# Kernel optimization log

Measured on AMD Instinct MI355X. Metric: run time of the kernel, lower is better.

## Reference

```python
import jax, jax.numpy as jnp
import numpy as np

N = 50000          # nodes
E = 500000         # edges
EMB = 64           # hidden_size
R = 2              # DDE num_rounds
RR = 2             # DDE num_reverse_rounds
PRED_IN = 4 * EMB + 4 + 4 * (R + RR)  # 276


def setup_inputs() -> dict:
    key = jax.random.key(0)
    ks = jax.random.split(key, 10)
    x = jax.random.normal(ks[0], (N, EMB), jnp.float32)
    edge_index = jax.random.randint(ks[1], (2, E), 0, N, dtype=jnp.int64)
    edge_attr = jax.random.normal(ks[2], (E, EMB), jnp.float32)
    topic_signal = jax.random.uniform(ks[3], (N, 2), dtype=jnp.float32)
    q_emb = jax.random.normal(ks[4], (E, EMB), jnp.float32)
    # learned parameters
    non_text_emb = jax.random.normal(ks[5], (1, EMB), jnp.float32)
    W1 = jax.random.normal(ks[6], (PRED_IN, EMB), jnp.float32) / np.sqrt(PRED_IN)
    b1 = jnp.zeros((EMB,), jnp.float32)
    W2 = jax.random.normal(ks[7], (EMB, 1), jnp.float32) / np.sqrt(EMB)
    b2 = jnp.zeros((1,), jnp.float32)
    return dict(x=x, edge_index=edge_index, edge_attr=edge_attr,
                topic_signal=topic_signal, q_emb=q_emb,
                non_text_emb=non_text_emb, W1=W1, b1=b1, W2=W2, b2=b2)


def _segment_mean(data, seg, num_segments):
    # mean aggregation as in PyG MessagePassing(aggr='mean'); empty segments -> 0
    s = jax.ops.segment_sum(data, seg, num_segments=num_segments)
    cnt = jax.ops.segment_sum(jnp.ones((seg.shape[0],), data.dtype), seg,
                              num_segments=num_segments)
    return s / jnp.maximum(cnt, 1.0)[:, None]


def reference(x, edge_index, edge_attr, topic_signal, q_emb,
              non_text_emb, W1, b1, W2, b2):
    src, dst = edge_index[0], edge_index[1]
    # replace all-zero node rows with the learned non-text entity embedding
    zero_mask = jnp.all(x == 0, axis=1)
    x = jnp.where(zero_mask[:, None], non_text_emb[0], x)

    feats = [x, topic_signal]  # topic_pe = True
    # DDE forward rounds: aggregate src -> dst along edge_index
    h = topic_signal
    for _ in range(R):
        h = _segment_mean(h[src], dst, N)
        feats.append(h)
    # DDE reverse rounds: flipped edges (dst -> src)
    h = topic_signal
    for _ in range(RR):
        h = _segment_mean(h[dst], src, N)
        feats.append(h)

    h_e = jnp.concatenate(feats, axis=1)                      # [N, EMB+2+2*(R+RR)]
    h_triple = jnp.concatenate([q_emb, h_e[src], edge_attr, h_e[dst]], axis=1)  # [E, PRED_IN]
    hidden = jax.nn.relu(h_triple @ W1 + b1)                  # [E, EMB]
    return (hidden @ W2 + b2).squeeze(-1)                     # [E]
```

## Files before the change

kernel.cpp:

```cpp
#include <hip/hip_runtime.h>
#include <cstdint>
#include <cstddef>


typedef __bf16 bf16x8 __attribute__((ext_vector_type(8)));
typedef float f32x4 __attribute__((ext_vector_type(4)));

__device__ __forceinline__ unsigned int f2bf1(float f) {
    unsigned int u = __float_as_uint(f);
    return (u + 0x7fffu + ((u >> 16) & 1u)) >> 16;
}
__device__ __forceinline__ unsigned int pk2(float a, float b) {
    return f2bf1(a) | (f2bf1(b) << 16);
}
__device__ __forceinline__ bf16x8 cvt8v(float4 a, float4 b) {
    bf16x8 r;
    r[0] = (__bf16)a.x; r[1] = (__bf16)a.y; r[2] = (__bf16)a.z; r[3] = (__bf16)a.w;
    r[4] = (__bf16)b.x; r[5] = (__bf16)b.y; r[6] = (__bf16)b.z; r[7] = (__bf16)b.w;
    return r;
}

#define GL16(gp, lp)                                                        \
    __builtin_amdgcn_global_load_lds(                                       \
        (const __attribute__((address_space(1))) void*)(gp),                \
        (__attribute__((address_space(3))) void*)(lp), 16, 0, 0)


__global__ void k_detect(const int* __restrict__ idx, int E, int* __restrict__ flag) {
    int e = blockIdx.x * blockDim.x + threadIdx.x;
    bool nz = (e < E) && (idx[2 * e + 1] != 0);
    unsigned long long m = __ballot(nz);
    if (m != 0ull && (threadIdx.x & 63) == 0) atomicOr(flag, 1);
}

__global__ void k_convert(const int* __restrict__ idx, int E, const int* __restrict__ flag,
                          int* __restrict__ src_i, int* __restrict__ dst_i,
                          int* __restrict__ cnt_dst, int* __restrict__ cnt_src,
                          unsigned short* __restrict__ pos_f, unsigned short* __restrict__ pos_r) {
    int e = blockIdx.x * blockDim.x + threadIdx.x;
    if (e >= E) return;
    int s, d;
    if (*flag) { s = idx[e];     d = idx[E + e]; }
    else       { s = idx[2 * e]; d = idx[2 * E + 2 * e]; }
    src_i[e] = s; dst_i[e] = d;
    pos_f[e] = (unsigned short)atomicAdd(&cnt_dst[d], 1);
    pos_r[e] = (unsigned short)atomicAdd(&cnt_src[s], 1);
}

__global__ void k_scan(const int* __restrict__ cnt_dst, const int* __restrict__ cnt_src,
                       int* __restrict__ off_f, int* __restrict__ off_r, int N) {
    const int* cnt = (blockIdx.x == 0) ? cnt_dst : cnt_src;
    int* off       = (blockIdx.x == 0) ? off_f   : off_r;
    const int t = threadIdx.x;
    const int C = (N + 1023) / 1024;
    int lo = t * C, hi = lo + C; if (hi > N) hi = N; if (lo > N) lo = N;
    int sum = 0;
    for (int i = lo; i < hi; ++i) sum += cnt[i];
    __shared__ int wsum[16];
    int lane = t & 63, wv = t >> 6;
    int v = sum;
    for (int ofs = 1; ofs < 64; ofs <<= 1) {
        int u = __shfl_up(v, ofs);
        if (lane >= ofs) v += u;
    }
    if (lane == 63) wsum[wv] = v;
    __syncthreads();
    if (wv == 0) {
        int x = (lane < 16) ? wsum[lane] : 0;
        for (int ofs = 1; ofs < 16; ofs <<= 1) {
            int u = __shfl_up(x, ofs);
            if (lane >= ofs) x += u;
        }
        if (lane < 16) wsum[lane] = x;
    }
    __syncthreads();
    int base = (wv > 0 ? wsum[wv - 1] : 0) + (v - sum);
    for (int i = lo; i < hi; ++i) { off[i] = base; base += cnt[i]; }
}

__global__ void k_fill(const int* __restrict__ src_i, const int* __restrict__ dst_i,
                       const unsigned short* __restrict__ pos_f, const unsigned short* __restrict__ pos_r,
                       const int* __restrict__ off_f, const int* __restrict__ off_r,
                       int* __restrict__ csr_f, int* __restrict__ csr_r, int E) {
    int e = blockIdx.x * blockDim.x + threadIdx.x;
    if (e >= E) return;
    int s = src_i[e], d = dst_i[e];
    csr_f[off_f[d] + pos_f[e]] = s;
    csr_r[off_r[s] + pos_r[e]] = d;
}

__global__ void k_round(const int* __restrict__ off_f, const int* __restrict__ csr_f,
                        const int* __restrict__ off_r, const int* __restrict__ csr_r,
                        const float* __restrict__ hf_in,
                        const float* __restrict__ hr_in,
                        float* __restrict__ f_out, float* __restrict__ r_out,
                        int N, int E) {
    int gid = blockIdx.x * blockDim.x + threadIdx.x;
    if (gid >= 2 * N) return;
    const bool rev = gid >= N;
    const int n = rev ? gid - N : gid;
    const int* __restrict__ off = rev ? off_r : off_f;
    const int* __restrict__ csr = rev ? csr_r : csr_f;
    const float2* __restrict__ h = (const float2*)(rev ? hr_in : hf_in);
    float2* __restrict__ o = (float2*)(rev ? r_out : f_out);
    int b = off[n], e = (n + 1 < N) ? off[n + 1] : E;
    float sx = 0.f, sy = 0.f;
    for (int j = b; j < e; ++j) { float2 t = h[csr[j]]; sx += t.x; sy += t.y; }
    float inv = 1.0f / (float)max(e - b, 1);
    o[n] = make_float2(sx * inv, sy * inv);
}

__global__ void k_build(const float* __restrict__ x, const float* __restrict__ topic,
                        const float* __restrict__ nte,
                        const float* __restrict__ f1, const float* __restrict__ f2,
                        const float* __restrict__ r1, const float* __restrict__ r2,
                        unsigned short* __restrict__ he, int N) {
    int n = blockIdx.x * blockDim.x + threadIdx.x;
    if (n >= N) return;
    const float4* xr = (const float4*)(x + (size_t)n * 64);
    float4 v[16];
    bool allz = true;
#pragma unroll
    for (int i = 0; i < 16; ++i) {
        v[i] = xr[i];
        allz = allz && (v[i].x == 0.f && v[i].y == 0.f && v[i].z == 0.f && v[i].w == 0.f);
    }
    const float4* nr = (const float4*)nte;
    unsigned int row[40];
#pragma unroll
    for (int i = 0; i < 16; ++i) {
        float4 s = allz ? nr[i] : v[i];
        row[2 * i]     = pk2(s.x, s.y);
        row[2 * i + 1] = pk2(s.z, s.w);
    }
    row[32] = pk2(topic[2 * n], topic[2 * n + 1]);
    row[33] = pk2(f1[2 * n], f1[2 * n + 1]);
    row[34] = pk2(f2[2 * n], f2[2 * n + 1]);
    row[35] = pk2(r1[2 * n], r1[2 * n + 1]);
    row[36] = pk2(r2[2 * n], r2[2 * n + 1]);
    row[37] = 0u; row[38] = 0u; row[39] = 0u;
    uint4* dst = (uint4*)(he + (size_t)n * 80);
#pragma unroll
    for (int i = 0; i < 10; ++i) dst[i] = ((const uint4*)row)[i];
}

__global__ void k_w1t(const float* __restrict__ W1, unsigned short* __restrict__ W1T) {
    int i = blockIdx.x * blockDim.x + threadIdx.x;
    if (i >= 64 * 288) return;
    int j = i & 7;
    int l = (i >> 3) & 63;
    int t36 = i >> 9;
    int ks = t36 % 9, ct = t36 / 9;
    int col = ct * 16 + (l & 15);
    int pk = ks * 32 + (l >> 4) * 8 + j;
    int k = 0; bool valid = true;
    if (pk < 64)       { k = pk; }
    else if (pk < 128) { k = 138 + (pk - 64); }
    else if (pk < 208) { int jj = pk - 128; k = 64 + jj;  valid = jj < 74; }
    else               { int jj = pk - 208; k = 202 + jj; valid = jj < 74; }
    float v = valid ? W1[k * 64 + col] : 0.f;
    W1T[i] = (unsigned short)f2bf1(v);
}


__launch_bounds__(256, 2)
__global__ void k_gemm(const float* __restrict__ q_emb,
                       const float* __restrict__ edge_attr,
                       const unsigned short* __restrict__ he,
                       const unsigned short* __restrict__ W1Tg,
                       const int* __restrict__ src_i, const int* __restrict__ dst_i,
                       const float* __restrict__ b1, const float* __restrict__ W2,
                       const float* __restrict__ b2, float* __restrict__ out, int E)
{
    __shared__ __align__(64) char smem[77824];
    const int tid = threadIdx.x;
    const int w = tid >> 6, l = tid & 63, c = l & 15, q = l >> 4;
    const int NW = gridDim.x * 4;
    const int gw = blockIdx.x * 4 + w;
    const int ntiles = E / 16;

#pragma unroll
    for (int jj = 0; jj < 9; ++jj) {
        int j = w * 9 + jj;
        GL16((const char*)W1Tg + j * 1024 + l * 16, smem + j * 1024);
    }

    char* buf0 = smem + 36864 + w * 10240;
    char* buf1 = buf0 + 5120;

    int T = gw;
    {
        int e0 = T * 16 + c;
        int s0 = src_i[e0], d0 = dst_i[e0];
#pragma unroll
        for (int j = 0; j < 5; ++j) {
            int ch = j * 4 + q;
            int node = ch < 10 ? s0 : d0;
            int chunk = ch < 10 ? ch : ch - 10;
            GL16((const char*)he + (size_t)node * 160 + chunk * 16, buf0 + j * 1024);
        }
    }
    const float* qr0 = q_emb     + (size_t)(T * 16 + c) * 64 + q * 8;
    const float* ar0 = edge_attr + (size_t)(T * 16 + c) * 64 + q * 8;
    float4 qc0 = *(const float4*)qr0,        qc1 = *(const float4*)(qr0 + 4);
    float4 qc2 = *(const float4*)(qr0 + 32), qc3 = *(const float4*)(qr0 + 36);
    float4 ec0 = *(const float4*)ar0,        ec1 = *(const float4*)(ar0 + 4);
    float4 ec2 = *(const float4*)(ar0 + 32), ec3 = *(const float4*)(ar0 + 36);
    int siA, diA, siB, diB;
    {
        int eA = min(T + NW, ntiles - 1) * 16 + c;
        int eB = min(T + 2 * NW, ntiles - 1) * 16 + c;
        siA = src_i[eA]; diA = dst_i[eA];
        siB = src_i[eB]; diB = dst_i[eB];
    }
    float b1v[4], w2v[4];
#pragma unroll
    for (int ct = 0; ct < 4; ++ct) { b1v[ct] = b1[ct * 16 + c]; w2v[ct] = W2[ct * 16 + c]; }
    const float bb = b2[0];
    __syncthreads();

    int cur = 0;
    while (T < ntiles) {
        const int Tn = T + NW;
        const bool more = Tn < ntiles;
        float4 qn0, qn1, qn2, qn3, en0, en1, en2, en3;
        int siC = siB, diC = diB;
        char* sbuf = cur ? buf0 : buf1;
        char* cbuf = cur ? buf1 : buf0;

        if (more) {
            const float* qr = q_emb     + (size_t)(Tn * 16 + c) * 64 + q * 8;
            const float* ar = edge_attr + (size_t)(Tn * 16 + c) * 64 + q * 8;
            qn0 = *(const float4*)qr;        qn1 = *(const float4*)(qr + 4);
            qn2 = *(const float4*)(qr + 32); qn3 = *(const float4*)(qr + 36);
            en0 = *(const float4*)ar;        en1 = *(const float4*)(ar + 4);
            en2 = *(const float4*)(ar + 32); en3 = *(const float4*)(ar + 36);
#pragma unroll
            for (int j = 0; j < 5; ++j) {
                int ch = j * 4 + q;
                int node = ch < 10 ? siA : diA;
                int chunk = ch < 10 ? ch : ch - 10;
                GL16((const char*)he + (size_t)node * 160 + chunk * 16, sbuf + j * 1024);
            }
            int eC = min(T + 3 * NW, ntiles - 1) * 16 + c;
            siC = src_i[eC]; diC = dst_i[eC];
            asm volatile("s_waitcnt vmcnt(15)" ::: "memory");
        } else {
            qn0 = qc0; qn1 = qc1; qn2 = qc2; qn3 = qc3;
            en0 = ec0; en1 = ec1; en2 = ec2; en3 = ec3;
            asm volatile("s_waitcnt vmcnt(0)" ::: "memory");
        }
        __builtin_amdgcn_sched_barrier(0);

        f32x4 acc0 = {}, acc1 = {}, acc2 = {}, acc3 = {};
        const char* wbase = smem + (size_t)l * 16;
#define BF(ct, ks) (*(const bf16x8*)(wbase + (ct) * 9216 + (ks) * 1024))
#define HEF(pl) (*(const bf16x8*)(cbuf + (pl) * 256 + c * 16))
#define KST(ks, A)                                                                 \
        {                                                                          \
            bf16x8 a_ = (A);                                                       \
            acc0 = __builtin_amdgcn_mfma_f32_16x16x32_bf16(a_, BF(0, ks), acc0, 0, 0, 0); \
            acc1 = __builtin_amdgcn_mfma_f32_16x16x32_bf16(a_, BF(1, ks), acc1, 0, 0, 0); \
            acc2 = __builtin_amdgcn_mfma_f32_16x16x32_bf16(a_, BF(2, ks), acc2, 0, 0, 0); \
            acc3 = __builtin_amdgcn_mfma_f32_16x16x32_bf16(a_, BF(3, ks), acc3, 0, 0, 0); \
        }
        KST(0, cvt8v(qc0, qc1))
        KST(1, cvt8v(qc2, qc3))
        KST(2, cvt8v(ec0, ec1))
        KST(3, cvt8v(ec2, ec3))
        KST(4, HEF(q))
        KST(5, HEF(q + 4))
        KST(6, HEF(q + 8))
        KST(7, HEF(q + 12))
        KST(8, HEF(q + 16))
#undef KST
#undef HEF
#undef BF

        float pr[4];
#pragma unroll
        for (int r = 0; r < 4; ++r) {
            float h0 = fmaxf(acc0[r] + b1v[0], 0.f);
            float h1 = fmaxf(acc1[r] + b1v[1], 0.f);
            float h2 = fmaxf(acc2[r] + b1v[2], 0.f);
            float h3 = fmaxf(acc3[r] + b1v[3], 0.f);
            float p = fmaf(h0, w2v[0], fmaf(h1, w2v[1], fmaf(h2, w2v[2], h3 * w2v[3])));
            p += __shfl_xor(p, 1);
            p += __shfl_xor(p, 2);
            p += __shfl_xor(p, 4);
            p += __shfl_xor(p, 8);
            pr[r] = p;
        }
        if (c == 0) {
            *(float4*)&out[T * 16 + q * 4] =
                make_float4(pr[0] + bb, pr[1] + bb, pr[2] + bb, pr[3] + bb);
        }

        qc0 = qn0; qc1 = qn1; qc2 = qn2; qc3 = qn3;
        ec0 = en0; ec1 = en1; ec2 = en2; ec3 = en3;
        siA = siB; diA = diB; siB = siC; diB = diC;
        T = Tn; cur ^= 1;
    }
}


extern "C" void kernel_launch(void* const* d_in, const int* in_sizes, int n_in,
                              void* d_out, int out_size, void* d_ws, size_t ws_size,
                              hipStream_t stream)
{
    const float* x         = (const float*)d_in[0];
    const int*   eidx      = (const int*)  d_in[1];
    const float* edge_attr = (const float*)d_in[2];
    const float* topic     = (const float*)d_in[3];
    const float* q_emb     = (const float*)d_in[4];
    const float* nte       = (const float*)d_in[5];
    const float* W1        = (const float*)d_in[6];
    const float* b1        = (const float*)d_in[7];
    const float* W2        = (const float*)d_in[8];
    const float* b2        = (const float*)d_in[9];
    float* out = (float*)d_out;

    const int E = out_size;
    const int N = in_sizes[0] / 64;

    char* ws = (char*)d_ws;
    int* flag  = (int*)ws;
    int* src_i = (int*)(ws + 16);
    int* dst_i = src_i + E;
    int* off_f = dst_i + E;
    int* off_r = off_f + N;
    float* fblk = (float*)(off_r + N);
    float* f1 = fblk;
    float* f2 = fblk + 2 * (size_t)N;
    float* r1 = fblk + 4 * (size_t)N;
    float* r2 = fblk + 6 * (size_t)N;
    int* cnt_dst = (int*)f1;
    int* cnt_src = cnt_dst + N;
    char* heblk = (char*)(fblk + 8 * (size_t)N);
    unsigned short* pos_f = (unsigned short*)heblk;
    unsigned short* pos_r = pos_f + E;
    int* csr_f = (int*)(pos_r + E);
    int* csr_r = csr_f + E;
    unsigned short* he = (unsigned short*)heblk;
    size_t he_bytes = (size_t)N * 160;
    size_t trans_bytes = (size_t)E * 12;
    size_t heblk_bytes = he_bytes > trans_bytes ? he_bytes : trans_bytes;
    unsigned short* W1T = (unsigned short*)(heblk + heblk_bytes);

    size_t needed = 16 + (size_t)8 * E + (size_t)8 * N + (size_t)32 * N + heblk_bytes + 64 * 288 * 2;
    if (ws_size < needed) return;

    hipMemsetAsync(flag, 0, 16, stream);
    hipMemsetAsync(cnt_dst, 0, (size_t)8 * N, stream);

    const int gE = (E + 255) / 256;
    const int gN = (N + 255) / 256;
    const int gN2 = (2 * N + 255) / 256;

    k_detect <<<gE, 256, 0, stream>>>(eidx, E, flag);
    k_convert<<<gE, 256, 0, stream>>>(eidx, E, flag, src_i, dst_i,
                                      cnt_dst, cnt_src, pos_f, pos_r);
    k_scan   <<<2, 1024, 0, stream>>>(cnt_dst, cnt_src, off_f, off_r, N);
    k_fill   <<<gE, 256, 0, stream>>>(src_i, dst_i, pos_f, pos_r, off_f, off_r,
                                      csr_f, csr_r, E);
    k_round  <<<gN2, 256, 0, stream>>>(off_f, csr_f, off_r, csr_r, topic, topic, f1, r1, N, E);
    k_round  <<<gN2, 256, 0, stream>>>(off_f, csr_f, off_r, csr_r, f1, r1, f2, r2, N, E);
    k_build  <<<gN, 256, 0, stream>>>(x, topic, nte, f1, f2, r1, r2, he, N);
    k_w1t    <<<(64 * 288 + 255) / 256, 256, 0, stream>>>(W1, W1T);

    k_gemm<<<512, 256, 0, stream>>>(q_emb, edge_attr, he, W1T,
                                    src_i, dst_i, b1, W2, b2, out, E);
}
```

Baseline: 554.8 us.

## Deepen gemm prefetch to triple-buffered gathers and fold W1 transpose into detect

The gemm kernel now uses 512-thread blocks (8 waves) and half as many blocks, which shares the LDS copy of W1 across more waves. It prefetches two tiles ahead through a three-slot LDS ring for the gathered node features and keeps two tiles of q_emb/edge_attr in registers, so more memory latency is hidden. The W1 transpose kernel is merged into k_detect as extra blocks, removing one launch. The cost is more register and LDS pressure (about 156 KB of LDS per block), which may limit occupancy to a single block per CU.

```diff
diff --git a/kernel.cpp b/kernel.cpp
--- a/kernel.cpp
+++ b/kernel.cpp
@@ -26,7 +26,27 @@
         (__attribute__((address_space(3))) void*)(lp), 16, 0, 0)
 
 
-__global__ void k_detect(const int* __restrict__ idx, int E, int* __restrict__ flag) {
+__global__ void k_detect(const int* __restrict__ idx, int E, int* __restrict__ flag,
+                         int gE, const float* __restrict__ W1,
+                         unsigned short* __restrict__ W1T) {
+    if ((int)blockIdx.x >= gE) {
+        int i = (blockIdx.x - gE) * blockDim.x + threadIdx.x;
+        if (i >= 64 * 288) return;
+        int j = i & 7;
+        int l = (i >> 3) & 63;
+        int t36 = i >> 9;
+        int ks = t36 % 9, ct = t36 / 9;
+        int col = ct * 16 + (l & 15);
+        int pk = ks * 32 + (l >> 4) * 8 + j;
+        int k = 0; bool valid = true;
+        if (pk < 64)       { k = pk; }
+        else if (pk < 128) { k = 138 + (pk - 64); }
+        else if (pk < 208) { int jj = pk - 128; k = 64 + jj;  valid = jj < 74; }
+        else               { int jj = pk - 208; k = 202 + jj; valid = jj < 74; }
+        float v = valid ? W1[k * 64 + col] : 0.f;
+        W1T[i] = (unsigned short)f2bf1(v);
+        return;
+    }
     int e = blockIdx.x * blockDim.x + threadIdx.x;
     bool nz = (e < E) && (idx[2 * e + 1] != 0);
     unsigned long long m = __ballot(nz);
@@ -144,26 +164,8 @@
     for (int i = 0; i < 10; ++i) dst[i] = ((const uint4*)row)[i];
 }
 
-__global__ void k_w1t(const float* __restrict__ W1, unsigned short* __restrict__ W1T) {
-    int i = blockIdx.x * blockDim.x + threadIdx.x;
-    if (i >= 64 * 288) return;
-    int j = i & 7;
-    int l = (i >> 3) & 63;
-    int t36 = i >> 9;
-    int ks = t36 % 9, ct = t36 / 9;
-    int col = ct * 16 + (l & 15);
-    int pk = ks * 32 + (l >> 4) * 8 + j;
-    int k = 0; bool valid = true;
-    if (pk < 64)       { k = pk; }
-    else if (pk < 128) { k = 138 + (pk - 64); }
-    else if (pk < 208) { int jj = pk - 128; k = 64 + jj;  valid = jj < 74; }
-    else               { int jj = pk - 208; k = 202 + jj; valid = jj < 74; }
-    float v = valid ? W1[k * 64 + col] : 0.f;
-    W1T[i] = (unsigned short)f2bf1(v);
-}
-
-
-__launch_bounds__(256, 2)
+
+__launch_bounds__(512, 2)
 __global__ void k_gemm(const float* __restrict__ q_emb,
                        const float* __restrict__ edge_attr,
                        const unsigned short* __restrict__ he,
@@ -172,86 +174,96 @@
                        const float* __restrict__ b1, const float* __restrict__ W2,
                        const float* __restrict__ b2, float* __restrict__ out, int E)
 {
-    __shared__ __align__(64) char smem[77824];
+    __shared__ __align__(64) char smem[159744];
     const int tid = threadIdx.x;
     const int w = tid >> 6, l = tid & 63, c = l & 15, q = l >> 4;
-    const int NW = gridDim.x * 4;
-    const int gw = blockIdx.x * 4 + w;
+    const int NW = gridDim.x * 8;
+    const int gw = blockIdx.x * 8 + w;
     const int ntiles = E / 16;
 
-#pragma unroll
-    for (int jj = 0; jj < 9; ++jj) {
-        int j = w * 9 + jj;
+    for (int j = w; j < 36; j += 8) {
         GL16((const char*)W1Tg + j * 1024 + l * 16, smem + j * 1024);
     }
 
-    char* buf0 = smem + 36864 + w * 10240;
-    char* buf1 = buf0 + 5120;
+    char* bufb = smem + 36864 + w * 15360;
+
+#define EIDX(t) ((((t) < ntiles) ? (t) : (ntiles - 1)) * 16 + c)
 
     int T = gw;
     {
-        int e0 = T * 16 + c;
-        int s0 = src_i[e0], d0 = dst_i[e0];
+        int e0 = EIDX(T);        int s0 = src_i[e0], d0 = dst_i[e0];
+        int e1 = EIDX(T + NW);   int s1 = src_i[e1], d1 = dst_i[e1];
 #pragma unroll
         for (int j = 0; j < 5; ++j) {
             int ch = j * 4 + q;
-            int node = ch < 10 ? s0 : d0;
-            int chunk = ch < 10 ? ch : ch - 10;
-            GL16((const char*)he + (size_t)node * 160 + chunk * 16, buf0 + j * 1024);
-        }
-    }
-    const float* qr0 = q_emb     + (size_t)(T * 16 + c) * 64 + q * 8;
-    const float* ar0 = edge_attr + (size_t)(T * 16 + c) * 64 + q * 8;
+            int nsel0 = ch < 10 ? s0 : d0; int ck = ch < 10 ? ch : ch - 10;
+            int nsel1 = ch < 10 ? s1 : d1;
+            GL16((const char*)he + (size_t)nsel0 * 160 + ck * 16, bufb + j * 1024);
+            GL16((const char*)he + (size_t)nsel1 * 160 + ck * 16, bufb + 5120 + j * 1024);
+        }
+    }
+    const float* qr0 = q_emb     + (size_t)EIDX(T) * 64 + q * 8;
+    const float* ar0 = edge_attr + (size_t)EIDX(T) * 64 + q * 8;
     float4 qc0 = *(const float4*)qr0,        qc1 = *(const float4*)(qr0 + 4);
     float4 qc2 = *(const float4*)(qr0 + 32), qc3 = *(const float4*)(qr0 + 36);
     float4 ec0 = *(const float4*)ar0,        ec1 = *(const float4*)(ar0 + 4);
     float4 ec2 = *(const float4*)(ar0 + 32), ec3 = *(const float4*)(ar0 + 36);
-    int siA, diA, siB, diB;
-    {
-        int eA = min(T + NW, ntiles - 1) * 16 + c;
-        int eB = min(T + 2 * NW, ntiles - 1) * 16 + c;
-        siA = src_i[eA]; diA = dst_i[eA];
-        siB = src_i[eB]; diB = dst_i[eB];
-    }
+    const float* qr1 = q_emb     + (size_t)EIDX(T + NW) * 64 + q * 8;
+    const float* ar1 = edge_attr + (size_t)EIDX(T + NW) * 64 + q * 8;
+    float4 q10 = *(const float4*)qr1,        q11 = *(const float4*)(qr1 + 4);
+    float4 q12 = *(const float4*)(qr1 + 32), q13 = *(const float4*)(qr1 + 36);
+    float4 e10 = *(const float4*)ar1,        e11 = *(const float4*)(ar1 + 4);
+    float4 e12 = *(const float4*)(ar1 + 32), e13 = *(const float4*)(ar1 + 36);
+    int si2, di2, si3, di3, si4, di4;
+    { int e = EIDX(T + 2 * NW); si2 = src_i[e]; di2 = dst_i[e]; }
+    { int e = EIDX(T + 3 * NW); si3 = src_i[e]; di3 = dst_i[e]; }
+    { int e = EIDX(T + 4 * NW); si4 = src_i[e]; di4 = dst_i[e]; }
+
     float b1v[4], w2v[4];
 #pragma unroll
     for (int ct = 0; ct < 4; ++ct) { b1v[ct] = b1[ct * 16 + c]; w2v[ct] = W2[ct * 16 + c]; }
     const float bb = b2[0];
     __syncthreads();
 
-    int cur = 0;
+    int rc = 0;
     while (T < ntiles) {
-        const int Tn = T + NW;
-        const bool more = Tn < ntiles;
-        float4 qn0, qn1, qn2, qn3, en0, en1, en2, en3;
-        int siC = siB, diC = diB;
-        char* sbuf = cur ? buf0 : buf1;
-        char* cbuf = cur ? buf1 : buf0;
-
-        if (more) {
-            const float* qr = q_emb     + (size_t)(Tn * 16 + c) * 64 + q * 8;
-            const float* ar = edge_attr + (size_t)(Tn * 16 + c) * 64 + q * 8;
-            qn0 = *(const float4*)qr;        qn1 = *(const float4*)(qr + 4);
-            qn2 = *(const float4*)(qr + 32); qn3 = *(const float4*)(qr + 36);
-            en0 = *(const float4*)ar;        en1 = *(const float4*)(ar + 4);
-            en2 = *(const float4*)(ar + 32); en3 = *(const float4*)(ar + 36);
+        const bool more1 = (T + NW) < ntiles;
+        const bool more2 = (T + 2 * NW) < ntiles;
+        float4 q20, q21, q22, q23, e20, e21, e22, e23;
+        int sin = si3, din = di3;
+
+        if (more2) {
+            const int Tp = T + 2 * NW;
+            const float* qr = q_emb     + (size_t)(Tp * 16 + c) * 64 + q * 8;
+            const float* ar = edge_attr + (size_t)(Tp * 16 + c) * 64 + q * 8;
+            q20 = *(const float4*)qr;        q21 = *(const float4*)(qr + 4);
+            q22 = *(const float4*)(qr + 32); q23 = *(const float4*)(qr + 36);
+            e20 = *(const float4*)ar;        e21 = *(const float4*)(ar + 4);
+            e22 = *(const float4*)(ar + 32); e23 = *(const float4*)(ar + 36);
+            int rs = rc + 2; rs = rs >= 3 ? rs - 3 : rs;
+            char* sbuf = bufb + rs * 5120;
 #pragma unroll
             for (int j = 0; j < 5; ++j) {
                 int ch = j * 4 + q;
-                int node = ch < 10 ? siA : diA;
-                int chunk = ch < 10 ? ch : ch - 10;
-                GL16((const char*)he + (size_t)node * 160 + chunk * 16, sbuf + j * 1024);
+                int node = ch < 10 ? si2 : di2;
+                int ck = ch < 10 ? ch : ch - 10;
+                GL16((const char*)he + (size_t)node * 160 + ck * 16, sbuf + j * 1024);
             }
-            int eC = min(T + 3 * NW, ntiles - 1) * 16 + c;
-            siC = src_i[eC]; diC = dst_i[eC];
+            int ep = EIDX(T + 5 * NW);
+            sin = src_i[ep]; din = dst_i[ep];
+            asm volatile("s_waitcnt vmcnt(30)" ::: "memory");
+        } else if (more1) {
+            q20 = qc0; q21 = qc1; q22 = qc2; q23 = qc3;
+            e20 = ec0; e21 = ec1; e22 = ec2; e23 = ec3;
             asm volatile("s_waitcnt vmcnt(15)" ::: "memory");
         } else {
-            qn0 = qc0; qn1 = qc1; qn2 = qc2; qn3 = qc3;
-            en0 = ec0; en1 = ec1; en2 = ec2; en3 = ec3;
+            q20 = qc0; q21 = qc1; q22 = qc2; q23 = qc3;
+            e20 = ec0; e21 = ec1; e22 = ec2; e23 = ec3;
             asm volatile("s_waitcnt vmcnt(0)" ::: "memory");
         }
         __builtin_amdgcn_sched_barrier(0);
 
+        char* cbuf = bufb + rc * 5120;
         f32x4 acc0 = {}, acc1 = {}, acc2 = {}, acc3 = {};
         const char* wbase = smem + (size_t)l * 16;
 #define BF(ct, ks) (*(const bf16x8*)(wbase + (ct) * 9216 + (ks) * 1024))
@@ -296,11 +308,15 @@
                 make_float4(pr[0] + bb, pr[1] + bb, pr[2] + bb, pr[3] + bb);
         }
 
-        qc0 = qn0; qc1 = qn1; qc2 = qn2; qc3 = qn3;
-        ec0 = en0; ec1 = en1; ec2 = en2; ec3 = en3;
-        siA = siB; diA = diB; siB = siC; diB = diC;
-        T = Tn; cur ^= 1;
-    }
+        qc0 = q10; qc1 = q11; qc2 = q12; qc3 = q13;
+        ec0 = e10; ec1 = e11; ec2 = e12; ec3 = e13;
+        q10 = q20; q11 = q21; q12 = q22; q13 = q23;
+        e10 = e20; e11 = e21; e12 = e22; e13 = e23;
+        si2 = si3; di2 = di3; si3 = si4; di3 = di4; si4 = sin; di4 = din;
+        rc = rc == 2 ? 0 : rc + 1;
+        T += NW;
+    }
+#undef EIDX
 }
 
 
@@ -356,8 +372,9 @@
     const int gE = (E + 255) / 256;
     const int gN = (N + 255) / 256;
     const int gN2 = (2 * N + 255) / 256;
-
-    k_detect <<<gE, 256, 0, stream>>>(eidx, E, flag);
+    const int gW = (64 * 288 + 255) / 256;
+
+    k_detect <<<gE + gW, 256, 0, stream>>>(eidx, E, flag, gE, W1, W1T);
     k_convert<<<gE, 256, 0, stream>>>(eidx, E, flag, src_i, dst_i,
                                       cnt_dst, cnt_src, pos_f, pos_r);
     k_scan   <<<2, 1024, 0, stream>>>(cnt_dst, cnt_src, off_f, off_r, N);
@@ -366,8 +383,7 @@
     k_round  <<<gN2, 256, 0, stream>>>(off_f, csr_f, off_r, csr_r, topic, topic, f1, r1, N, E);
     k_round  <<<gN2, 256, 0, stream>>>(off_f, csr_f, off_r, csr_r, f1, r1, f2, r2, N, E);
     k_build  <<<gN, 256, 0, stream>>>(x, topic, nte, f1, f2, r1, r2, he, N);
-    k_w1t    <<<(64 * 288 + 255) / 256, 256, 0, stream>>>(W1, W1T);
-
-    k_gemm<<<512, 256, 0, stream>>>(q_emb, edge_attr, he, W1T,
+
+    k_gemm<<<256, 512, 0, stream>>>(q_emb, edge_attr, he, W1T,
                                     src_i, dst_i, b1, W2, b2, out, E);
 }
```

Result: no change. 554.9 us (+0.0%).

## Fuse graph preprocessing into one cooperative kernel with a parallel scan

Applied to the files above, without the earlier changes.

The detect, convert, scan, fill, two DDE rounds, node-row build and W1 transpose kernels are merged into one cooperative kernel of 256 blocks × 1024 threads. Stages are separated by grid-wide syncs, which removes seven kernel launches and the gaps between them. The two-block serial prefix scan becomes a two-level scan spread across all blocks, with per-block totals kept in scratch space aliased onto the r2 buffer. In exchange it adds grid-sync cost, needs co-residency of all 256 large blocks, and uses grid-stride loops that may leave fewer threads for the gather-heavy rounds.

```diff
diff --git a/kernel.cpp b/kernel.cpp
--- a/kernel.cpp
+++ b/kernel.cpp
@@ -1,6 +1,9 @@
 #include <hip/hip_runtime.h>
+#include <hip/hip_cooperative_groups.h>
 #include <cstdint>
 #include <cstddef>
+
+namespace cg = cooperative_groups;
 
 
 typedef __bf16 bf16x8 __attribute__((ext_vector_type(8)));
@@ -26,140 +29,184 @@
         (__attribute__((address_space(3))) void*)(lp), 16, 0, 0)
 
 
-__global__ void k_detect(const int* __restrict__ idx, int E, int* __restrict__ flag) {
-    int e = blockIdx.x * blockDim.x + threadIdx.x;
-    bool nz = (e < E) && (idx[2 * e + 1] != 0);
-    unsigned long long m = __ballot(nz);
-    if (m != 0ull && (threadIdx.x & 63) == 0) atomicOr(flag, 1);
-}
-
-__global__ void k_convert(const int* __restrict__ idx, int E, const int* __restrict__ flag,
-                          int* __restrict__ src_i, int* __restrict__ dst_i,
-                          int* __restrict__ cnt_dst, int* __restrict__ cnt_src,
-                          unsigned short* __restrict__ pos_f, unsigned short* __restrict__ pos_r) {
-    int e = blockIdx.x * blockDim.x + threadIdx.x;
-    if (e >= E) return;
-    int s, d;
-    if (*flag) { s = idx[e];     d = idx[E + e]; }
-    else       { s = idx[2 * e]; d = idx[2 * E + 2 * e]; }
-    src_i[e] = s; dst_i[e] = d;
-    pos_f[e] = (unsigned short)atomicAdd(&cnt_dst[d], 1);
-    pos_r[e] = (unsigned short)atomicAdd(&cnt_src[s], 1);
-}
-
-__global__ void k_scan(const int* __restrict__ cnt_dst, const int* __restrict__ cnt_src,
-                       int* __restrict__ off_f, int* __restrict__ off_r, int N) {
-    const int* cnt = (blockIdx.x == 0) ? cnt_dst : cnt_src;
-    int* off       = (blockIdx.x == 0) ? off_f   : off_r;
+__device__ __forceinline__ void round_body(int gtid, int gsz, int N, int E,
+                                           const int* __restrict__ off_f,
+                                           const int* __restrict__ csr_f,
+                                           const int* __restrict__ off_r,
+                                           const int* __restrict__ csr_r,
+                                           const float2* __restrict__ hf,
+                                           const float2* __restrict__ hr,
+                                           float2* __restrict__ fo,
+                                           float2* __restrict__ ro) {
+    for (int gid = gtid; gid < 2 * N; gid += gsz) {
+        const bool rev = gid >= N;
+        const int n = rev ? gid - N : gid;
+        const int* __restrict__ off = rev ? off_r : off_f;
+        const int* __restrict__ csr = rev ? csr_r : csr_f;
+        const float2* __restrict__ h = rev ? hr : hf;
+        int b = off[n], e = (n + 1 < N) ? off[n + 1] : E;
+        float sx = 0.f, sy = 0.f;
+        for (int j = b; j < e; ++j) { float2 t = h[csr[j]]; sx += t.x; sy += t.y; }
+        float inv = 1.0f / (float)max(e - b, 1);
+        (rev ? ro : fo)[n] = make_float2(sx * inv, sy * inv);
+    }
+}
+
+__launch_bounds__(1024)
+__global__ void k_prep(const int* __restrict__ idx, int E, int N,
+                       int* __restrict__ flag,
+                       const float* __restrict__ W1, unsigned short* __restrict__ W1T,
+                       int* __restrict__ src_i, int* __restrict__ dst_i,
+                       int* __restrict__ cnt_dst, int* __restrict__ cnt_src,
+                       unsigned short* __restrict__ pos_f, unsigned short* __restrict__ pos_r,
+                       int* __restrict__ off_f, int* __restrict__ off_r,
+                       int* __restrict__ csr_f, int* __restrict__ csr_r,
+                       int* __restrict__ totf, int* __restrict__ totr,
+                       const float* __restrict__ topic, const float* __restrict__ x,
+                       const float* __restrict__ nte,
+                       float* __restrict__ f1, float* __restrict__ f2,
+                       float* __restrict__ r1, float* __restrict__ r2,
+                       unsigned short* __restrict__ he)
+{
+    cg::grid_group grid = cg::this_grid();
+    __shared__ int wp[16];
+
     const int t = threadIdx.x;
-    const int C = (N + 1023) / 1024;
-    int lo = t * C, hi = lo + C; if (hi > N) hi = N; if (lo > N) lo = N;
-    int sum = 0;
-    for (int i = lo; i < hi; ++i) sum += cnt[i];
-    __shared__ int wsum[16];
-    int lane = t & 63, wv = t >> 6;
-    int v = sum;
-    for (int ofs = 1; ofs < 64; ofs <<= 1) {
-        int u = __shfl_up(v, ofs);
-        if (lane >= ofs) v += u;
-    }
-    if (lane == 63) wsum[wv] = v;
-    __syncthreads();
-    if (wv == 0) {
-        int x = (lane < 16) ? wsum[lane] : 0;
-        for (int ofs = 1; ofs < 16; ofs <<= 1) {
-            int u = __shfl_up(x, ofs);
-            if (lane >= ofs) x += u;
-        }
-        if (lane < 16) wsum[lane] = x;
-    }
-    __syncthreads();
-    int base = (wv > 0 ? wsum[wv - 1] : 0) + (v - sum);
-    for (int i = lo; i < hi; ++i) { off[i] = base; base += cnt[i]; }
-}
-
-__global__ void k_fill(const int* __restrict__ src_i, const int* __restrict__ dst_i,
-                       const unsigned short* __restrict__ pos_f, const unsigned short* __restrict__ pos_r,
-                       const int* __restrict__ off_f, const int* __restrict__ off_r,
-                       int* __restrict__ csr_f, int* __restrict__ csr_r, int E) {
-    int e = blockIdx.x * blockDim.x + threadIdx.x;
-    if (e >= E) return;
-    int s = src_i[e], d = dst_i[e];
-    csr_f[off_f[d] + pos_f[e]] = s;
-    csr_r[off_r[s] + pos_r[e]] = d;
-}
-
-__global__ void k_round(const int* __restrict__ off_f, const int* __restrict__ csr_f,
-                        const int* __restrict__ off_r, const int* __restrict__ csr_r,
-                        const float* __restrict__ hf_in,
-                        const float* __restrict__ hr_in,
-                        float* __restrict__ f_out, float* __restrict__ r_out,
-                        int N, int E) {
-    int gid = blockIdx.x * blockDim.x + threadIdx.x;
-    if (gid >= 2 * N) return;
-    const bool rev = gid >= N;
-    const int n = rev ? gid - N : gid;
-    const int* __restrict__ off = rev ? off_r : off_f;
-    const int* __restrict__ csr = rev ? csr_r : csr_f;
-    const float2* __restrict__ h = (const float2*)(rev ? hr_in : hf_in);
-    float2* __restrict__ o = (float2*)(rev ? r_out : f_out);
-    int b = off[n], e = (n + 1 < N) ? off[n + 1] : E;
-    float sx = 0.f, sy = 0.f;
-    for (int j = b; j < e; ++j) { float2 t = h[csr[j]]; sx += t.x; sy += t.y; }
-    float inv = 1.0f / (float)max(e - b, 1);
-    o[n] = make_float2(sx * inv, sy * inv);
-}
-
-__global__ void k_build(const float* __restrict__ x, const float* __restrict__ topic,
-                        const float* __restrict__ nte,
-                        const float* __restrict__ f1, const float* __restrict__ f2,
-                        const float* __restrict__ r1, const float* __restrict__ r2,
-                        unsigned short* __restrict__ he, int N) {
-    int n = blockIdx.x * blockDim.x + threadIdx.x;
-    if (n >= N) return;
-    const float4* xr = (const float4*)(x + (size_t)n * 64);
-    float4 v[16];
-    bool allz = true;
-#pragma unroll
-    for (int i = 0; i < 16; ++i) {
-        v[i] = xr[i];
-        allz = allz && (v[i].x == 0.f && v[i].y == 0.f && v[i].z == 0.f && v[i].w == 0.f);
-    }
-    const float4* nr = (const float4*)nte;
-    unsigned int row[40];
-#pragma unroll
-    for (int i = 0; i < 16; ++i) {
-        float4 s = allz ? nr[i] : v[i];
-        row[2 * i]     = pk2(s.x, s.y);
-        row[2 * i + 1] = pk2(s.z, s.w);
-    }
-    row[32] = pk2(topic[2 * n], topic[2 * n + 1]);
-    row[33] = pk2(f1[2 * n], f1[2 * n + 1]);
-    row[34] = pk2(f2[2 * n], f2[2 * n + 1]);
-    row[35] = pk2(r1[2 * n], r1[2 * n + 1]);
-    row[36] = pk2(r2[2 * n], r2[2 * n + 1]);
-    row[37] = 0u; row[38] = 0u; row[39] = 0u;
-    uint4* dst = (uint4*)(he + (size_t)n * 80);
-#pragma unroll
-    for (int i = 0; i < 10; ++i) dst[i] = ((const uint4*)row)[i];
-}
-
-__global__ void k_w1t(const float* __restrict__ W1, unsigned short* __restrict__ W1T) {
-    int i = blockIdx.x * blockDim.x + threadIdx.x;
-    if (i >= 64 * 288) return;
-    int j = i & 7;
-    int l = (i >> 3) & 63;
-    int t36 = i >> 9;
-    int ks = t36 % 9, ct = t36 / 9;
-    int col = ct * 16 + (l & 15);
-    int pk = ks * 32 + (l >> 4) * 8 + j;
-    int k = 0; bool valid = true;
-    if (pk < 64)       { k = pk; }
-    else if (pk < 128) { k = 138 + (pk - 64); }
-    else if (pk < 208) { int jj = pk - 128; k = 64 + jj;  valid = jj < 74; }
-    else               { int jj = pk - 208; k = 202 + jj; valid = jj < 74; }
-    float v = valid ? W1[k * 64 + col] : 0.f;
-    W1T[i] = (unsigned short)f2bf1(v);
+    const int b = blockIdx.x;
+    const int nb = gridDim.x;
+    const int gsz = nb * 1024;
+    const int gtid = b * 1024 + t;
+    const int lane = t & 63;
+    const int wid = t >> 6;
+
+    for (int e = gtid; e < E; e += gsz) {
+        bool nz = idx[2 * e + 1] != 0;
+        unsigned long long m = __ballot(nz);
+        if (m != 0ull && lane == 0) atomicOr(flag, 1);
+    }
+    for (int i = gtid; i < 64 * 288; i += gsz) {
+        int j = i & 7;
+        int l = (i >> 3) & 63;
+        int t36 = i >> 9;
+        int ks = t36 % 9, ct = t36 / 9;
+        int col = ct * 16 + (l & 15);
+        int pk = ks * 32 + (l >> 4) * 8 + j;
+        int k = 0; bool valid = true;
+        if (pk < 64)       { k = pk; }
+        else if (pk < 128) { k = 138 + (pk - 64); }
+        else if (pk < 208) { int jj = pk - 128; k = 64 + jj;  valid = jj < 74; }
+        else               { int jj = pk - 208; k = 202 + jj; valid = jj < 74; }
+        float v = valid ? W1[k * 64 + col] : 0.f;
+        W1T[i] = (unsigned short)f2bf1(v);
+    }
+    grid.sync();
+
+    {
+        const int fl = *flag;
+        for (int e = gtid; e < E; e += gsz) {
+            int s, d;
+            if (fl) { s = idx[e];     d = idx[E + e]; }
+            else    { s = idx[2 * e]; d = idx[2 * E + 2 * e]; }
+            src_i[e] = s; dst_i[e] = d;
+            pos_f[e] = (unsigned short)atomicAdd(&cnt_dst[d], 1);
+            pos_r[e] = (unsigned short)atomicAdd(&cnt_src[s], 1);
+        }
+    }
+    grid.sync();
+
+    const int C = (N + nb - 1) / nb;
+    const int grp = t >> 8;
+    const int u = t & 255;
+    int pref = 0;
+    {
+        int i = b * C + u;
+        int val = 0;
+        if (grp < 2 && u < C && i < N) val = (grp == 0 ? cnt_dst : cnt_src)[i];
+        int incl = val;
+        for (int ofs = 1; ofs < 64; ofs <<= 1) {
+            int uu = __shfl_up(incl, ofs);
+            if (lane >= ofs) incl += uu;
+        }
+        if (lane == 63) wp[wid] = incl;
+        __syncthreads();
+        int wofs = 0;
+        if (grp < 2) {
+            int base = grp * 4, wi = wid - base;
+            for (int k = 0; k < wi; ++k) wofs += wp[base + k];
+        }
+        pref = wofs + incl - val;
+        if (grp < 2 && u == 255) (grp == 0 ? totf : totr)[b] = wofs + incl;
+    }
+    grid.sync();
+
+    if (b == 0) {
+        int val = 0;
+        if (grp < 2 && u < nb) val = (grp == 0 ? totf : totr)[u];
+        int incl = val;
+        for (int ofs = 1; ofs < 64; ofs <<= 1) {
+            int uu = __shfl_up(incl, ofs);
+            if (lane >= ofs) incl += uu;
+        }
+        __syncthreads();
+        if (lane == 63) wp[wid] = incl;
+        __syncthreads();
+        int wofs = 0;
+        if (grp < 2) {
+            int base = grp * 4, wi = wid - base;
+            for (int k = 0; k < wi; ++k) wofs += wp[base + k];
+        }
+        if (grp < 2 && u < nb) (grp == 0 ? totf : totr)[u] = wofs + incl - val;
+    }
+    grid.sync();
+
+    {
+        int i = b * C + u;
+        if (grp == 0 && u < C && i < N) off_f[i] = totf[b] + pref;
+        if (grp == 1 && u < C && i < N) off_r[i] = totr[b] + pref;
+    }
+    grid.sync();
+
+    for (int e = gtid; e < E; e += gsz) {
+        int s = src_i[e], d = dst_i[e];
+        csr_f[off_f[d] + pos_f[e]] = s;
+        csr_r[off_r[s] + pos_r[e]] = d;
+    }
+    grid.sync();
+
+    round_body(gtid, gsz, N, E, off_f, csr_f, off_r, csr_r,
+               (const float2*)topic, (const float2*)topic, (float2*)f1, (float2*)r1);
+    grid.sync();
+    round_body(gtid, gsz, N, E, off_f, csr_f, off_r, csr_r,
+               (const float2*)f1, (const float2*)r1, (float2*)f2, (float2*)r2);
+    grid.sync();
+
+    for (int n = gtid; n < N; n += gsz) {
+        const float4* xr = (const float4*)(x + (size_t)n * 64);
+        float4 v[16];
+        bool allz = true;
+#pragma unroll
+        for (int i = 0; i < 16; ++i) {
+            v[i] = xr[i];
+            allz = allz && (v[i].x == 0.f && v[i].y == 0.f && v[i].z == 0.f && v[i].w == 0.f);
+        }
+        const float4* nr = (const float4*)nte;
+        unsigned int row[40];
+#pragma unroll
+        for (int i = 0; i < 16; ++i) {
+            float4 s = allz ? nr[i] : v[i];
+            row[2 * i]     = pk2(s.x, s.y);
+            row[2 * i + 1] = pk2(s.z, s.w);
+        }
+        row[32] = pk2(topic[2 * n], topic[2 * n + 1]);
+        row[33] = pk2(f1[2 * n], f1[2 * n + 1]);
+        row[34] = pk2(f2[2 * n], f2[2 * n + 1]);
+        row[35] = pk2(r1[2 * n], r1[2 * n + 1]);
+        row[36] = pk2(r2[2 * n], r2[2 * n + 1]);
+        row[37] = 0u; row[38] = 0u; row[39] = 0u;
+        uint4* dst = (uint4*)(he + (size_t)n * 80);
+#pragma unroll
+        for (int i = 0; i < 10; ++i) dst[i] = ((const uint4*)row)[i];
+    }
 }
 
 
@@ -336,6 +383,8 @@
     float* r2 = fblk + 6 * (size_t)N;
     int* cnt_dst = (int*)f1;
     int* cnt_src = cnt_dst + N;
+    int* totf = (int*)r2;
+    int* totr = totf + 256;
     char* heblk = (char*)(fblk + 8 * (size_t)N);
     unsigned short* pos_f = (unsigned short*)heblk;
     unsigned short* pos_r = pos_f + E;
@@ -353,20 +402,18 @@
     hipMemsetAsync(flag, 0, 16, stream);
     hipMemsetAsync(cnt_dst, 0, (size_t)8 * N, stream);
 
-    const int gE = (E + 255) / 256;
-    const int gN = (N + 255) / 256;
-    const int gN2 = (2 * N + 255) / 256;
-
-    k_detect <<<gE, 256, 0, stream>>>(eidx, E, flag);
-    k_convert<<<gE, 256, 0, stream>>>(eidx, E, flag, src_i, dst_i,
-                                      cnt_dst, cnt_src, pos_f, pos_r);
-    k_scan   <<<2, 1024, 0, stream>>>(cnt_dst, cnt_src, off_f, off_r, N);
-    k_fill   <<<gE, 256, 0, stream>>>(src_i, dst_i, pos_f, pos_r, off_f, off_r,
-                                      csr_f, csr_r, E);
-    k_round  <<<gN2, 256, 0, stream>>>(off_f, csr_f, off_r, csr_r, topic, topic, f1, r1, N, E);
-    k_round  <<<gN2, 256, 0, stream>>>(off_f, csr_f, off_r, csr_r, f1, r1, f2, r2, N, E);
-    k_build  <<<gN, 256, 0, stream>>>(x, topic, nte, f1, f2, r1, r2, he, N);
-    k_w1t    <<<(64 * 288 + 255) / 256, 256, 0, stream>>>(W1, W1T);
+    int Ei = E, Ni = N;
+    void* args[] = {
+        (void*)&eidx, (void*)&Ei, (void*)&Ni, (void*)&flag,
+        (void*)&W1, (void*)&W1T,
+        (void*)&src_i, (void*)&dst_i, (void*)&cnt_dst, (void*)&cnt_src,
+        (void*)&pos_f, (void*)&pos_r, (void*)&off_f, (void*)&off_r,
+        (void*)&csr_f, (void*)&csr_r, (void*)&totf, (void*)&totr,
+        (void*)&topic, (void*)&x, (void*)&nte,
+        (void*)&f1, (void*)&f2, (void*)&r1, (void*)&r2, (void*)&he
+    };
+    hipLaunchCooperativeKernel((const void*)k_prep, dim3(256), dim3(1024),
+                               args, 0, stream);
 
     k_gemm<<<512, 256, 0, stream>>>(q_emb, edge_attr, he, W1T,
                                     src_i, dst_i, b1, W2, b2, out, E);
```

Result: slower. 722.4 us (+30.2%).
